# Kernel optimization log

Hardware: AMD Instinct MI355X
Metric: run time of the kernel (lower is better)

## Reference

```python
import jax, jax.numpy as jnp
import numpy as np

D = 512
H = 8
DH = D // H
HID = int(2 * D * 4.0 * (2.0 / 3.0))  # 2730, SwiGLU hidden


def _ln(x, g, b, eps=1e-5):
    m = jnp.mean(x, axis=-1, keepdims=True)
    v = jnp.mean(jnp.square(x - m), axis=-1, keepdims=True)
    return (x - m) * jax.lax.rsqrt(v + eps) * g + b


def _cross_attn(q_tok, kv_tok, ln_q_g, ln_q_b, ln_kv_g, ln_kv_b,
                Wqkv, bqkv, Wo, bo, Wp, bp):
    # q_tok: [B,Nq,D], kv_tok: [B,Nk,D]; Wqkv: [3D,D] fused in_proj (torch layout)
    B, Nq, _ = q_tok.shape
    Nk = kv_tok.shape[1]
    qn = _ln(q_tok, ln_q_g, ln_q_b)
    kvn = _ln(kv_tok, ln_kv_g, ln_kv_b)
    Wq, Wk, Wv = Wqkv[:D], Wqkv[D:2 * D], Wqkv[2 * D:]
    bq, bk, bv = bqkv[:D], bqkv[D:2 * D], bqkv[2 * D:]
    q = (qn @ Wq.T + bq).reshape(B, Nq, H, DH).transpose(0, 2, 1, 3)
    k = (kvn @ Wk.T + bk).reshape(B, Nk, H, DH).transpose(0, 2, 1, 3)
    v = (kvn @ Wv.T + bv).reshape(B, Nk, H, DH).transpose(0, 2, 1, 3)
    scores = jnp.einsum('bhqd,bhkd->bhqk', q, k) / jnp.sqrt(jnp.asarray(DH, q.dtype))
    attn = jax.nn.softmax(scores, axis=-1)
    ctx = jnp.einsum('bhqk,bhkd->bhqd', attn, v)
    ctx = ctx.transpose(0, 2, 1, 3).reshape(B, Nq, D)
    ctx = ctx @ Wo.T + bo          # MHA out_proj
    ctx = ctx @ Wp.T + bp          # CrossAttention extra out_proj
    return q_tok + ctx             # residual (dropout/droppath identity in eval)


def setup_inputs() -> dict:
    key = jax.random.key(0)
    ks = iter(jax.random.split(key, 32))
    s = 0.02
    inp = {
        'spatial_tokens': jax.random.normal(next(ks), (4, 4096, D), jnp.float32),
        'temporal_tokens': jax.random.normal(next(ks), (4, 512, D), jnp.float32),
    }
    for p in ('s', 't'):
        inp[f'{p}_ln_q_g'] = jnp.ones((D,), jnp.float32)
        inp[f'{p}_ln_q_b'] = jnp.zeros((D,), jnp.float32)
        inp[f'{p}_ln_kv_g'] = jnp.ones((D,), jnp.float32)
        inp[f'{p}_ln_kv_b'] = jnp.zeros((D,), jnp.float32)
        inp[f'{p}_Wqkv'] = jax.random.normal(next(ks), (3 * D, D), jnp.float32) * s
        inp[f'{p}_bqkv'] = jnp.zeros((3 * D,), jnp.float32)
        inp[f'{p}_Wo'] = jax.random.normal(next(ks), (D, D), jnp.float32) * s
        inp[f'{p}_bo'] = jnp.zeros((D,), jnp.float32)
        inp[f'{p}_Wp'] = jax.random.normal(next(ks), (D, D), jnp.float32) * s
        inp[f'{p}_bp'] = jnp.zeros((D,), jnp.float32)
    inp['mix_ln_g'] = jnp.ones((2 * D,), jnp.float32)
    inp['mix_ln_b'] = jnp.zeros((2 * D,), jnp.float32)
    inp['mix_Win'] = jax.random.normal(next(ks), (2 * HID, 2 * D), jnp.float32) * s
    inp['mix_bin'] = jnp.zeros((2 * HID,), jnp.float32)
    inp['mix_Wout'] = jax.random.normal(next(ks), (D, HID), jnp.float32) * s
    inp['mix_bout'] = jnp.zeros((D,), jnp.float32)
    return inp


def reference(spatial_tokens, temporal_tokens,
              s_ln_q_g, s_ln_q_b, s_ln_kv_g, s_ln_kv_b, s_Wqkv, s_bqkv, s_Wo, s_bo, s_Wp, s_bp,
              t_ln_q_g, t_ln_q_b, t_ln_kv_g, t_ln_kv_b, t_Wqkv, t_bqkv, t_Wo, t_bo, t_Wp, t_bp,
              mix_ln_g, mix_ln_b, mix_Win, mix_bin, mix_Wout, mix_bout):
    # 'st' (spatiotemporal) mode of CrossTransformer.forward
    s_ctx = _cross_attn(spatial_tokens, temporal_tokens,
                        s_ln_q_g, s_ln_q_b, s_ln_kv_g, s_ln_kv_b,
                        s_Wqkv, s_bqkv, s_Wo, s_bo, s_Wp, s_bp)
    t_ctx = _cross_attn(temporal_tokens, spatial_tokens,
                        t_ln_q_g, t_ln_q_b, t_ln_kv_g, t_ln_kv_b,
                        t_Wqkv, t_bqkv, t_Wo, t_bo, t_Wp, t_bp)
    t_mean = jnp.mean(t_ctx, axis=1, keepdims=True)  # [B,1,D]
    base = jnp.concatenate([s_ctx, jnp.broadcast_to(t_mean, s_ctx.shape)], axis=-1)  # [B,Ns,2D]
    h = _ln(base, mix_ln_g, mix_ln_b)
    uv = h @ mix_Win.T + mix_bin            # [B,Ns,2*HID]
    u, v = uv[..., :HID], uv[..., HID:]
    fused = (jax.nn.silu(u) * v) @ mix_Wout.T + mix_bout
    return s_ctx + fused
```

## Files before the change

kernel.cpp:

```cpp
#include <hip/hip_runtime.h>
#include <stdint.h>

typedef unsigned short u16;
typedef __bf16 bf16_t;
typedef bf16_t bf16x8 __attribute__((ext_vector_type(8)));
typedef float f32x4 __attribute__((ext_vector_type(4)));

__device__ __forceinline__ u16 f2b(float f) {
  union { float f; uint32_t u; } x; x.f = f;
  uint32_t r = x.u + 0x7fffu + ((x.u >> 16) & 1u);
  return (u16)(r >> 16);
}
__device__ __forceinline__ float b2f(u16 b) {
  union { uint32_t u; float f; } x; x.u = ((uint32_t)b) << 16;
  return x.f;
}

__device__ __forceinline__ void async16(const void* g, void* l) {
  auto gp = reinterpret_cast<__attribute__((address_space(1))) unsigned int*>(
      reinterpret_cast<uintptr_t>(g));
  auto lp = reinterpret_cast<__attribute__((address_space(3))) unsigned int*>(
      reinterpret_cast<uintptr_t>(l));
  __builtin_amdgcn_global_load_lds(gp, lp, 16, 0, 0);
}

__global__ __launch_bounds__(256) void pz_gemm_bt(
    const u16* __restrict__ A, const u16* __restrict__ B,
    const float* __restrict__ bias,
    const u16* __restrict__ residB, const float* __restrict__ residF,
    u16* __restrict__ Cb, float* __restrict__ Cf,
    int M, int N, int K, int ldA, int ldB, int ldC, int ldR,
    long aSH, long bSH, long cSH, long rSH, float alpha)
{
  __shared__ __align__(16) u16 sA[128 * 32];
  __shared__ __align__(16) u16 sB[128 * 32];

  const int tid = threadIdx.x;
  const int wave = tid >> 6, lane = tid & 63;
  const int lr = lane & 15, lg = lane >> 4;
  const int wm = wave >> 1, wn = wave & 1;
  const int z = blockIdx.z;

  const u16* Ab = A + (long)z * aSH;
  const u16* Bb = B + (long)z * bSH;
  const int m0 = blockIdx.y * 128;
  const int n0 = blockIdx.x * 128;

  const int srow = tid >> 2;
  const int sgk = (tid & 3) ^ ((tid >> 3) & 3);
  int ar0 = m0 + srow;      if (ar0 > M - 1) ar0 = M - 1;
  int ar1 = m0 + 64 + srow; if (ar1 > M - 1) ar1 = M - 1;
  int br0 = n0 + srow;      if (br0 > N - 1) br0 = N - 1;
  int br1 = n0 + 64 + srow; if (br1 > N - 1) br1 = N - 1;
  const u16* aP0 = Ab + (long)ar0 * ldA + sgk * 8;
  const u16* aP1 = Ab + (long)ar1 * ldA + sgk * 8;
  const u16* bP0 = Bb + (long)br0 * ldB + sgk * 8;
  const u16* bP1 = Bb + (long)br1 * ldB + sgk * 8;
  u16* sAw0 = sA + wave * 512;
  u16* sAw1 = sA + 2048 + wave * 512;
  u16* sBw0 = sB + wave * 512;
  u16* sBw1 = sB + 2048 + wave * 512;

  const int swz = (lr >> 1) & 3;
  int aoff[4], boff[4];
#pragma unroll
  for (int i = 0; i < 4; ++i) {
    aoff[i] = (wm * 64 + i * 16 + lr) * 32 + ((lg ^ swz) * 8);
    boff[i] = (wn * 64 + i * 16 + lr) * 32 + ((lg ^ swz) * 8);
  }

  f32x4 acc[4][4] = {};
  const int kiters = K >> 5;
  for (int kt = 0; kt < kiters; ++kt) {
    const int k0 = kt << 5;
    __syncthreads();
    async16(aP0 + k0, sAw0);
    async16(aP1 + k0, sAw1);
    async16(bP0 + k0, sBw0);
    async16(bP1 + k0, sBw1);
    __builtin_amdgcn_s_waitcnt(0x0f70);
    __syncthreads();

    bf16x8 af[4], bfr[4];
#pragma unroll
    for (int i = 0; i < 4; ++i) af[i] = *(const bf16x8*)(sA + aoff[i]);
#pragma unroll
    for (int i = 0; i < 4; ++i) bfr[i] = *(const bf16x8*)(sB + boff[i]);
#pragma unroll
    for (int i = 0; i < 4; ++i)
#pragma unroll
      for (int j = 0; j < 4; ++j)
        acc[i][j] = __builtin_amdgcn_mfma_f32_16x16x32_bf16(af[i], bfr[j], acc[i][j], 0, 0, 0);
  }

  const long coff = (long)z * cSH;
  const long roff = (long)z * rSH;
#pragma unroll
  for (int j = 0; j < 4; ++j) {
    const int n = n0 + wn * 64 + j * 16 + lr;
    if (n < N) {
      const float bv = bias ? bias[n] : 0.0f;
#pragma unroll
      for (int i = 0; i < 4; ++i) {
        const int mb = m0 + wm * 64 + i * 16 + lg * 4;
#pragma unroll
        for (int r = 0; r < 4; ++r) {
          const int m = mb + r;
          float v = alpha * acc[i][j][r] + bv;
          const long ri = roff + (long)m * ldR + n;
          if (residB) v += b2f(residB[ri]);
          if (residF) v += residF[ri];
          const long ci = coff + (long)m * ldC + n;
          if (Cb) Cb[ci] = f2b(v);
          if (Cf) Cf[ci] = v;
        }
      }
    }
  }
}

__global__ __launch_bounds__(256) void pz_sattn(
    const u16* __restrict__ Q, const u16* __restrict__ K,
    const u16* __restrict__ V, u16* __restrict__ O)
{
  __shared__ __align__(16) u16 sQ[32 * 64];
  __shared__ __align__(16) u16 sK[512 * 32];
  __shared__ float redm[32][4];
  __shared__ float reds[32][4];

  const int tid = threadIdx.x;
  const int wave = tid >> 6, lane = tid & 63;
  const int lr = lane & 15, lg = lane >> 4;
  const int z = blockIdx.z;
  const int b = z >> 3, h = z & 7;
  const int q0 = blockIdx.x * 32;

  const u16* Qb = Q + (long)b * 4096 * 512 + h * 64;
  const u16* Kb = K + (long)b * 512 * 1024 + h * 64;
  const u16* Vb = V + ((long)b * 8 + h) * (64L * 512);
  u16* Ob = O + (long)b * 4096 * 512 + h * 64;

  {
    const int qrow = wave * 8 + (lane >> 3);
    const int qcol = ((lane & 7) ^ (lane >> 3)) * 8;
    async16(Qb + (long)(q0 + qrow) * 512 + qcol, sQ + wave * 512);
  }
  const int krow = wave * 16 + (lane >> 2);
  const int kcol = ((lane & 3) ^ ((lane >> 3) & 3)) * 8;
  const u16* kP = Kb + (long)krow * 1024 + kcol;

  f32x4 acc[8][2] = {};
#pragma unroll
  for (int kk = 0; kk < 2; ++kk) {
    __syncthreads();
#pragma unroll
    for (int s = 0; s < 8; ++s)
      async16(kP + kk * 32 + (long)s * 64 * 1024, sK + s * 2048 + wave * 512);
    __builtin_amdgcn_s_waitcnt(0x0f70);
    __syncthreads();

    bf16x8 kf[8], qf[2];
#pragma unroll
    for (int kb = 0; kb < 8; ++kb) {
      const int n = wave * 128 + kb * 16 + lr;
      kf[kb] = *(const bf16x8*)(sK + n * 32 + ((lg ^ ((lr >> 1) & 3)) * 8));
    }
#pragma unroll
    for (int nq = 0; nq < 2; ++nq) {
      const int r = nq * 16 + lr;
      qf[nq] = *(const bf16x8*)(sQ + r * 64 + (((kk * 4 + lg) ^ (r & 7)) * 8));
    }
#pragma unroll
    for (int kb = 0; kb < 8; ++kb)
#pragma unroll
      for (int nq = 0; nq < 2; ++nq)
        acc[kb][nq] = __builtin_amdgcn_mfma_f32_16x16x32_bf16(kf[kb], qf[nq], acc[kb][nq], 0, 0, 0);
  }

  float mx0, mx1;
  {
    float m0 = acc[0][0][0], m1 = acc[0][1][0];
#pragma unroll
    for (int kb = 0; kb < 8; ++kb)
#pragma unroll
      for (int rg = 0; rg < 4; ++rg) {
        m0 = fmaxf(m0, acc[kb][0][rg]);
        m1 = fmaxf(m1, acc[kb][1][rg]);
      }
    m0 = fmaxf(m0, __shfl_xor(m0, 16, 64)); m0 = fmaxf(m0, __shfl_xor(m0, 32, 64));
    m1 = fmaxf(m1, __shfl_xor(m1, 16, 64)); m1 = fmaxf(m1, __shfl_xor(m1, 32, 64));
    mx0 = m0; mx1 = m1;
  }
  if (lane < 16) { redm[lr][wave] = mx0; redm[16 + lr][wave] = mx1; }
  __syncthreads();
  float inv[2];
#pragma unroll
  for (int nq = 0; nq < 2; ++nq) {
    const int q = nq * 16 + lr;
    const float m = fmaxf(fmaxf(redm[q][0], redm[q][1]), fmaxf(redm[q][2], redm[q][3]));
    float s = 0.0f;
#pragma unroll
    for (int kb = 0; kb < 8; ++kb)
#pragma unroll
      for (int rg = 0; rg < 4; ++rg) {
        const float e = __expf(0.125f * (acc[kb][nq][rg] - m));
        acc[kb][nq][rg] = e;
        s += e;
      }
    s += __shfl_xor(s, 16, 64);
    s += __shfl_xor(s, 32, 64);
    if (lane < 16) reds[q][wave] = s;
  }
  __syncthreads();
#pragma unroll
  for (int nq = 0; nq < 2; ++nq) {
    const int q = nq * 16 + lr;
    inv[nq] = 1.0f / (reds[q][0] + reds[q][1] + reds[q][2] + reds[q][3]);
  }

#pragma unroll
  for (int nq = 0; nq < 2; ++nq) {
    const int q = nq * 16 + lr;
#pragma unroll
    for (int kb = 0; kb < 8; ++kb) {
      ushort4 w;
      w.x = f2b(acc[kb][nq][0] * inv[nq]);
      w.y = f2b(acc[kb][nq][1] * inv[nq]);
      w.z = f2b(acc[kb][nq][2] * inv[nq]);
      w.w = f2b(acc[kb][nq][3] * inv[nq]);
      const int c16 = wave * 16 + kb * 2 + (lg >> 1);
      const int byteoff = q * 1024 + ((c16 ^ (q & 7)) * 16) + (lg & 1) * 8;
      *(ushort4*)((char*)sK + byteoff) = w;
    }
  }
  __syncthreads();

  const u16* vp = Vb + (long)(wave * 16 + lr) * 512;
  f32x4 opv[2] = {};
#pragma unroll
  for (int ks = 0; ks < 16; ++ks) {
    const bf16x8 bv = *(const bf16x8*)(vp + ks * 32 + lg * 8);
    bf16x8 pf[2];
#pragma unroll
    for (int mi = 0; mi < 2; ++mi) {
      const int r = mi * 16 + lr;
      pf[mi] = *(const bf16x8*)((char*)sK + r * 1024 + (((ks * 4 + lg) ^ (lr & 7)) * 16));
    }
#pragma unroll
    for (int mi = 0; mi < 2; ++mi)
      opv[mi] = __builtin_amdgcn_mfma_f32_16x16x32_bf16(pf[mi], bv, opv[mi], 0, 0, 0);
  }
#pragma unroll
  for (int mi = 0; mi < 2; ++mi)
#pragma unroll
    for (int rg = 0; rg < 4; ++rg) {
      const int q = q0 + mi * 16 + lg * 4 + rg;
      Ob[(long)q * 512 + wave * 16 + lr] = f2b(opv[mi][rg]);
    }
}

__global__ __launch_bounds__(256) void pz_tattn(
    const u16* __restrict__ Q,
    const u16* __restrict__ K,
    const u16* __restrict__ VT,
    u16* __restrict__ O)
{
  __shared__ __align__(16) u16 sQ[32 * 64];
  __shared__ __align__(16) u16 sK[512 * 32];
  __shared__ float redm[32][4];
  __shared__ float reds[32][4];
  __shared__ float m_run[32], l_run[32], alpha_sh[32];

  const int tid = threadIdx.x;
  const int wave = tid >> 6, lane = tid & 63;
  const int lr = lane & 15, lg = lane >> 4;
  const int z = blockIdx.z;
  const int b = z >> 3, h = z & 7;
  const int q0 = blockIdx.x * 32;

  const u16* Qb = Q + (long)b * 512 * 512 + h * 64;
  const u16* Kb = K + (long)b * 4096 * 1024 + h * 64;
  const u16* Vb = VT + (long)b * 512 * 4096 + (long)h * 64 * 4096;
  u16* Ob = O + (long)b * 512 * 512 + h * 64;

  if (tid < 32) { m_run[tid] = -3.0e38f; l_run[tid] = 0.0f; }

  {
    const int qrow = wave * 8 + (lane >> 3);
    const int qcol = ((lane & 7) ^ (lane >> 3)) * 8;
    async16(Qb + (long)(q0 + qrow) * 512 + qcol, sQ + wave * 512);
  }
  const int krow = wave * 16 + (lane >> 2);
  const int kcol = ((lane & 3) ^ ((lane >> 3) & 3)) * 8;

  f32x4 opv[2] = {};

  for (int kt = 0; kt < 8; ++kt) {
    const u16* kP = Kb + ((long)kt * 512 + krow) * 1024 + kcol;
    f32x4 acc[8][2] = {};
#pragma unroll
    for (int kk = 0; kk < 2; ++kk) {
      __syncthreads();
#pragma unroll
      for (int s = 0; s < 8; ++s)
        async16(kP + kk * 32 + (long)s * 64 * 1024, sK + s * 2048 + wave * 512);
      __builtin_amdgcn_s_waitcnt(0x0f70);
      __syncthreads();

      bf16x8 kf[8], qf[2];
#pragma unroll
      for (int kb = 0; kb < 8; ++kb) {
        const int n = wave * 128 + kb * 16 + lr;
        kf[kb] = *(const bf16x8*)(sK + n * 32 + ((lg ^ ((lr >> 1) & 3)) * 8));
      }
#pragma unroll
      for (int nq = 0; nq < 2; ++nq) {
        const int r = nq * 16 + lr;
        qf[nq] = *(const bf16x8*)(sQ + r * 64 + (((kk * 4 + lg) ^ (r & 7)) * 8));
      }
#pragma unroll
      for (int kb = 0; kb < 8; ++kb)
#pragma unroll
        for (int nq = 0; nq < 2; ++nq)
          acc[kb][nq] = __builtin_amdgcn_mfma_f32_16x16x32_bf16(kf[kb], qf[nq], acc[kb][nq], 0, 0, 0);
    }

#pragma unroll
    for (int nq = 0; nq < 2; ++nq) {
      float m = acc[0][nq][0];
#pragma unroll
      for (int kb = 0; kb < 8; ++kb)
#pragma unroll
        for (int rg = 0; rg < 4; ++rg) m = fmaxf(m, acc[kb][nq][rg]);
      m = fmaxf(m, __shfl_xor(m, 16, 64));
      m = fmaxf(m, __shfl_xor(m, 32, 64));
      if (lane < 16) redm[nq * 16 + lr][wave] = m;
    }
    __syncthreads();

#pragma unroll
    for (int nq = 0; nq < 2; ++nq) {
      const int q = nq * 16 + lr;
      const float mt = fmaxf(fmaxf(redm[q][0], redm[q][1]), fmaxf(redm[q][2], redm[q][3]));
      const float mn = fmaxf(m_run[q], mt);
      float s = 0.0f;
#pragma unroll
      for (int kb = 0; kb < 8; ++kb)
#pragma unroll
        for (int rg = 0; rg < 4; ++rg) {
          const float e = __expf(0.125f * (acc[kb][nq][rg] - mn));
          acc[kb][nq][rg] = e;
          s += e;
        }
      s += __shfl_xor(s, 16, 64);
      s += __shfl_xor(s, 32, 64);
      if (lane < 16) reds[q][wave] = s;
    }
    __syncthreads();

    if (tid < 32) {
      const int q = tid;
      const float mt = fmaxf(fmaxf(redm[q][0], redm[q][1]), fmaxf(redm[q][2], redm[q][3]));
      const float mo = m_run[q];
      const float mn = fmaxf(mo, mt);
      const float al = __expf(0.125f * (mo - mn));
      l_run[q] = l_run[q] * al + (reds[q][0] + reds[q][1] + reds[q][2] + reds[q][3]);
      m_run[q] = mn;
      alpha_sh[q] = al;
    }
#pragma unroll
    for (int nq = 0; nq < 2; ++nq) {
      const int q = nq * 16 + lr;
#pragma unroll
      for (int kb = 0; kb < 8; ++kb) {
        ushort4 w;
        w.x = f2b(acc[kb][nq][0]);
        w.y = f2b(acc[kb][nq][1]);
        w.z = f2b(acc[kb][nq][2]);
        w.w = f2b(acc[kb][nq][3]);
        const int c16 = wave * 16 + kb * 2 + (lg >> 1);
        const int byteoff = q * 1024 + ((c16 ^ (q & 7)) * 16) + (lg & 1) * 8;
        *(ushort4*)((char*)sK + byteoff) = w;
      }
    }
    __syncthreads();

#pragma unroll
    for (int mi = 0; mi < 2; ++mi)
#pragma unroll
      for (int rg = 0; rg < 4; ++rg)
        opv[mi][rg] *= alpha_sh[mi * 16 + lg * 4 + rg];

    const u16* vp = Vb + (long)(wave * 16 + lr) * 4096 + kt * 512;
#pragma unroll
    for (int ks = 0; ks < 16; ++ks) {
      const bf16x8 bv = *(const bf16x8*)(vp + ks * 32 + lg * 8);
      bf16x8 pf[2];
#pragma unroll
      for (int mi = 0; mi < 2; ++mi) {
        const int r = mi * 16 + lr;
        pf[mi] = *(const bf16x8*)((char*)sK + r * 1024 + (((ks * 4 + lg) ^ (lr & 7)) * 16));
      }
#pragma unroll
      for (int mi = 0; mi < 2; ++mi)
        opv[mi] = __builtin_amdgcn_mfma_f32_16x16x32_bf16(pf[mi], bv, opv[mi], 0, 0, 0);
    }
  }

#pragma unroll
  for (int mi = 0; mi < 2; ++mi)
#pragma unroll
    for (int rg = 0; rg < 4; ++rg) {
      const int qr = mi * 16 + lg * 4 + rg;
      Ob[(long)(q0 + qr) * 512 + wave * 16 + lr] = f2b(opv[mi][rg] * (1.0f / l_run[qr]));
    }
}

__global__ __launch_bounds__(256) void pz_gemm_uvgate(
    const u16* __restrict__ A, const u16* __restrict__ Bu, const u16* __restrict__ Bv,
    const float* __restrict__ biasU, const float* __restrict__ biasV,
    u16* __restrict__ G, int M, int N, int K, int ldA, int ldB, int ldG, int Npad)
{
  __shared__ __align__(16) u16 sA[2][128 * 32];
  __shared__ __align__(16) u16 sU[2][64 * 32];
  __shared__ __align__(16) u16 sV[2][64 * 32];

  const int tid = threadIdx.x;
  const int wave = tid >> 6, lane = tid & 63;
  const int lr = lane & 15, lg = lane >> 4;
  const int wm = wave >> 1, wn = wave & 1;
  const int m0 = blockIdx.y * 128;
  const int n0 = blockIdx.x * 64;

  const int srow = tid >> 2;
  const int sgk = (tid & 3) ^ ((tid >> 3) & 3);
  int ar0 = m0 + srow;      if (ar0 > M - 1) ar0 = M - 1;
  int ar1 = m0 + 64 + srow; if (ar1 > M - 1) ar1 = M - 1;
  int br  = n0 + srow;      if (br  > N - 1) br  = N - 1;
  const u16* aP0 = A + (long)ar0 * ldA + sgk * 8;
  const u16* aP1 = A + (long)ar1 * ldA + sgk * 8;
  const u16* uP  = Bu + (long)br * ldB + sgk * 8;
  const u16* vP  = Bv + (long)br * ldB + sgk * 8;

  auto stage = [&](int buf, int k0) {
    u16* a = sA[buf];
    u16* u = sU[buf];
    u16* v = sV[buf];
    async16(aP0 + k0, a + wave * 512);
    async16(aP1 + k0, a + 2048 + wave * 512);
    async16(uP + k0, u + wave * 512);
    async16(vP + k0, v + wave * 512);
  };

  const int swz = (lr >> 1) & 3;
  int aoff[4], boff[2];
#pragma unroll
  for (int i = 0; i < 4; ++i) aoff[i] = (wm * 64 + i * 16 + lr) * 32 + ((lg ^ swz) * 8);
#pragma unroll
  for (int j = 0; j < 2; ++j) boff[j] = (wn * 32 + j * 16 + lr) * 32 + ((lg ^ swz) * 8);

  f32x4 aU[4][2] = {}, aV[4][2] = {};
  const int kiters = K >> 5;

  stage(0, 0);
  __builtin_amdgcn_s_waitcnt(0x0f70);
  __syncthreads();

  int cur = 0;
  for (int kt = 0; kt < kiters; ++kt) {
    if (kt + 1 < kiters) stage(cur ^ 1, (kt + 1) << 5);

    const u16* sAc = sA[cur];
    const u16* sUc = sU[cur];
    const u16* sVc = sV[cur];
    bf16x8 af[4], uf[2], vf[2];
#pragma unroll
    for (int i = 0; i < 4; ++i) af[i] = *(const bf16x8*)(sAc + aoff[i]);
#pragma unroll
    for (int j = 0; j < 2; ++j) uf[j] = *(const bf16x8*)(sUc + boff[j]);
#pragma unroll
    for (int j = 0; j < 2; ++j) vf[j] = *(const bf16x8*)(sVc + boff[j]);
#pragma unroll
    for (int i = 0; i < 4; ++i)
#pragma unroll
      for (int j = 0; j < 2; ++j) {
        aU[i][j] = __builtin_amdgcn_mfma_f32_16x16x32_bf16(af[i], uf[j], aU[i][j], 0, 0, 0);
        aV[i][j] = __builtin_amdgcn_mfma_f32_16x16x32_bf16(af[i], vf[j], aV[i][j], 0, 0, 0);
      }

    __builtin_amdgcn_s_waitcnt(0x0f70);
    __syncthreads();
    cur ^= 1;
  }

#pragma unroll
  for (int j = 0; j < 2; ++j) {
    const int n = n0 + wn * 32 + j * 16 + lr;
    if (n < N) {
      const float bu = biasU[n], bv = biasV[n];
#pragma unroll
      for (int i = 0; i < 4; ++i) {
        const int mb = m0 + wm * 64 + i * 16 + lg * 4;
#pragma unroll
        for (int r = 0; r < 4; ++r) {
          const float u = aU[i][j][r] + bu;
          const float v = aV[i][j][r] + bv;
          G[(long)(mb + r) * ldG + n] = f2b((u / (1.0f + __expf(-u))) * v);
        }
      }
    } else if (n < Npad) {
#pragma unroll
      for (int i = 0; i < 4; ++i) {
        const int mb = m0 + wm * 64 + i * 16 + lg * 4;
#pragma unroll
        for (int r = 0; r < 4; ++r) G[(long)(mb + r) * ldG + n] = 0;
      }
    }
  }
}

__global__ __launch_bounds__(256) void pz_ln(const float* __restrict__ X, u16* __restrict__ O)
{
  __shared__ float sm[4], sq[4];
  const int tid = threadIdx.x;
  const long row = blockIdx.x;
  const float* x = X + row * 512;
  float a = x[tid], b = x[tid + 256];
  float s = a + b, q = a * a + b * b;
#pragma unroll
  for (int m = 32; m >= 1; m >>= 1) { s += __shfl_xor(s, m, 64); q += __shfl_xor(q, m, 64); }
  if ((tid & 63) == 0) { sm[tid >> 6] = s; sq[tid >> 6] = q; }
  __syncthreads();
  s = sm[0] + sm[1] + sm[2] + sm[3];
  q = sq[0] + sq[1] + sq[2] + sq[3];
  const float mean = s * (1.0f / 512.0f);
  const float rstd = rsqrtf(q * (1.0f / 512.0f) - mean * mean + 1e-5f);
  O[row * 512 + tid]       = f2b((a - mean) * rstd);
  O[row * 512 + tid + 256] = f2b((b - mean) * rstd);
}

__global__ __launch_bounds__(256) void pz_mix_ln(
    const u16* __restrict__ SC, const float* __restrict__ TM,
    const float* __restrict__ g, const float* __restrict__ b, u16* __restrict__ H)
{
  __shared__ float sm[4], sq[4];
  const int tid = threadIdx.x;
  const long row = blockIdx.x;
  const int bb = (int)(row >> 12);
  const u16* x0 = SC + row * 512;
  const float* x1 = TM + (long)bb * 512;
  float v0 = b2f(x0[tid]), v1 = b2f(x0[tid + 256]);
  float v2 = x1[tid], v3 = x1[tid + 256];
  float s = v0 + v1 + v2 + v3;
  float q = v0 * v0 + v1 * v1 + v2 * v2 + v3 * v3;
#pragma unroll
  for (int m = 32; m >= 1; m >>= 1) { s += __shfl_xor(s, m, 64); q += __shfl_xor(q, m, 64); }
  if ((tid & 63) == 0) { sm[tid >> 6] = s; sq[tid >> 6] = q; }
  __syncthreads();
  s = sm[0] + sm[1] + sm[2] + sm[3];
  q = sq[0] + sq[1] + sq[2] + sq[3];
  const float mean = s * (1.0f / 1024.0f);
  const float rstd = rsqrtf(q * (1.0f / 1024.0f) - mean * mean + 1e-5f);
  u16* hr = H + row * 1024;
  hr[tid]       = f2b((v0 - mean) * rstd * g[tid]       + b[tid]);
  hr[tid + 256] = f2b((v1 - mean) * rstd * g[tid + 256] + b[tid + 256]);
  hr[tid + 512] = f2b((v2 - mean) * rstd * g[tid + 512] + b[tid + 512]);
  hr[tid + 768] = f2b((v3 - mean) * rstd * g[tid + 768] + b[tid + 768]);
}

__global__ __launch_bounds__(256) void pz_transpose(
    const u16* __restrict__ S, u16* __restrict__ D, int Nk, int ldS, int colBase)
{
  __shared__ u16 t[64][65];
  const int z = blockIdx.z;
  const int nk0 = blockIdx.x * 64;
  const int tid = threadIdx.x;
  for (int i = tid; i < 4096; i += 256) {
    int r = i >> 6, d = i & 63;
    t[r][d] = S[(long)(nk0 + r) * ldS + colBase + z * 64 + d];
  }
  __syncthreads();
  for (int i = tid; i < 4096; i += 256) {
    int d = i >> 6, c = i & 63;
    D[((long)z * 64 + d) * Nk + nk0 + c] = t[c][d];
  }
}

__global__ __launch_bounds__(256) void pz_transpose_f2b(
    const float* __restrict__ S, u16* __restrict__ D, int Nk, int ldS)
{
  __shared__ u16 t[64][65];
  const int z = blockIdx.z;
  const int nk0 = blockIdx.x * 64;
  const int tid = threadIdx.x;
  for (int i = tid; i < 4096; i += 256) {
    int r = i >> 6, d = i & 63;
    t[r][d] = f2b(S[(long)(nk0 + r) * ldS + z * 64 + d]);
  }
  __syncthreads();
  for (int i = tid; i < 4096; i += 256) {
    int d = i >> 6, c = i & 63;
    D[((long)z * 64 + d) * Nk + nk0 + c] = t[c][d];
  }
}

__global__ __launch_bounds__(256) void pz_f2b(const float* __restrict__ s, u16* __restrict__ d, int n)
{
  int i = blockIdx.x * 256 + threadIdx.x;
  if (i < n) d[i] = f2b(s[i]);
}

__global__ __launch_bounds__(256) void pz_fold_qkv(
    const float* __restrict__ Ws, const float* __restrict__ Wt,
    const float* __restrict__ bs, const float* __restrict__ bt,
    const float* s_qg, const float* s_qb, const float* s_kg, const float* s_kb,
    const float* t_qg, const float* t_qb, const float* t_kg, const float* t_kb,
    u16* __restrict__ Wps, u16* __restrict__ Wpt, float* bps, float* bpt)
{
  __shared__ float sb[4];
  const int id = blockIdx.x;
  const int mat = (id >= 1536) ? 1 : 0;
  const int r = id - mat * 1536;
  const float* W = mat ? Wt : Ws;
  const float* bq = mat ? bt : bs;
  const float *g, *bl;
  if (!mat) { g = (r < 512) ? s_qg : s_kg; bl = (r < 512) ? s_qb : s_kb; }
  else      { g = (r < 512) ? t_qg : t_kg; bl = (r < 512) ? t_qb : t_kb; }
  u16* Wo_ = mat ? Wpt : Wps;
  float* bo_ = mat ? bpt : bps;
  float dot = 0.0f;
  for (int c = threadIdx.x; c < 512; c += 256) {
    float w = W[(long)r * 512 + c];
    Wo_[(long)r * 512 + c] = f2b(w * g[c]);
    dot += w * bl[c];
  }
#pragma unroll
  for (int m = 32; m >= 1; m >>= 1) dot += __shfl_xor(dot, m, 64);
  if ((threadIdx.x & 63) == 0) sb[threadIdx.x >> 6] = dot;
  __syncthreads();
  if (threadIdx.x == 0) bo_[r] = sb[0] + sb[1] + sb[2] + sb[3] + bq[r];
}

__global__ __launch_bounds__(256) void pz_fold_bc(
    const float* Wps_, const float* bos, const float* bps_,
    const float* Wpt_, const float* bot, const float* bpt_, float* bcs, float* bct)
{
  __shared__ float sb[4];
  const int id = blockIdx.x;
  const int mat = id >> 9, i = id & 511;
  const float* W = mat ? Wpt_ : Wps_;
  const float* bo = mat ? bot : bos;
  const float* bp = mat ? bpt_ : bps_;
  float* o = mat ? bct : bcs;
  float dot = 0.0f;
  for (int j = threadIdx.x; j < 512; j += 256) dot += W[(long)i * 512 + j] * bo[j];
#pragma unroll
  for (int m = 32; m >= 1; m >>= 1) dot += __shfl_xor(dot, m, 64);
  if ((threadIdx.x & 63) == 0) sb[threadIdx.x >> 6] = dot;
  __syncthreads();
  if (threadIdx.x == 0) o[i] = sb[0] + sb[1] + sb[2] + sb[3] + bp[i];
}

__global__ __launch_bounds__(256) void pz_pad_wout(const float* __restrict__ W, u16* __restrict__ D)
{
  const int idx = blockIdx.x * 256 + threadIdx.x;
  const int r = idx / 2816, c = idx - r * 2816;
  D[idx] = (c < 2730) ? f2b(W[(long)r * 2730 + c]) : (u16)0;
}

__global__ __launch_bounds__(256) void pz_tmean(const u16* __restrict__ T, float* __restrict__ O)
{
  const int b = blockIdx.y, tc = blockIdx.x, tid = threadIdx.x;
  const u16* base = T + (long)b * 512 * 512 + (long)tc * 32 * 512;
  float s0 = 0.0f, s1 = 0.0f;
#pragma unroll 4
  for (int t = 0; t < 32; ++t) { s0 += b2f(base[t * 512 + tid]); s1 += b2f(base[t * 512 + tid + 256]); }
  atomicAdd(&O[b * 512 + tid],       s0 * (1.0f / 512.0f));
  atomicAdd(&O[b * 512 + tid + 256], s1 * (1.0f / 512.0f));
}

__global__ void pz_diag(float* __restrict__ out, long n, float val)
{
  for (long i = (long)blockIdx.x * 256 + threadIdx.x; i < n; i += (long)gridDim.x * 256)
    out[i] = val;
}

extern "C" void kernel_launch(void* const* d_in, const int* in_sizes, int n_in,
                              void* d_out, int out_size, void* d_ws, size_t ws_size,
                              hipStream_t stream)
{
  (void)in_sizes; (void)n_in;
  const float* spat   = (const float*)d_in[0];
  const float* temp   = (const float*)d_in[1];
  const float* s_qg = (const float*)d_in[2],  * s_qb = (const float*)d_in[3];
  const float* s_kg = (const float*)d_in[4],  * s_kb = (const float*)d_in[5];
  const float* s_Wqkv = (const float*)d_in[6], * s_bqkv = (const float*)d_in[7];
  const float* s_Wo = (const float*)d_in[8],  * s_bo = (const float*)d_in[9];
  const float* s_Wp = (const float*)d_in[10], * s_bp = (const float*)d_in[11];
  const float* t_qg = (const float*)d_in[12], * t_qb = (const float*)d_in[13];
  const float* t_kg = (const float*)d_in[14], * t_kb = (const float*)d_in[15];
  const float* t_Wqkv = (const float*)d_in[16], * t_bqkv = (const float*)d_in[17];
  const float* t_Wo = (const float*)d_in[18], * t_bo = (const float*)d_in[19];
  const float* t_Wp = (const float*)d_in[20], * t_bp = (const float*)d_in[21];
  const float* mix_g = (const float*)d_in[22], * mix_b = (const float*)d_in[23];
  const float* mix_Win = (const float*)d_in[24], * mix_bin = (const float*)d_in[25];
  const float* mix_Wout = (const float*)d_in[26], * mix_bout = (const float*)d_in[27];
  float* out = (float*)d_out;

  char* ws = (char*)d_ws;
  size_t off = 0;
  auto take = [&](size_t n) { void* p = ws + off; off += (n + 255) & ~(size_t)255; return p; };

  u16* wq_s  = (u16*)take(1536L * 512 * 2);
  u16* wq_t  = (u16*)take(1536L * 512 * 2);
  u16* wc_s  = (u16*)take(512L * 512 * 2);
  u16* wc_t  = (u16*)take(512L * 512 * 2);
  u16* woutp = (u16*)take(512L * 2816 * 2);
  float* bqs = (float*)take(1536L * 4);
  float* bqt = (float*)take(1536L * 4);
  float* bcs = (float*)take(512L * 4);
  float* bct = (float*)take(512L * 4);
  u16* nhat_s = (u16*)take(16384L * 512 * 2);
  u16* nhat_t = (u16*)take(2048L * 512 * 2);
  u16* q_s  = (u16*)take(16384L * 512 * 2);
  u16* kv_s = (u16*)take(2048L * 1024 * 2);
  u16* q_t  = (u16*)take(2048L * 512 * 2);
  u16* kv_t = (u16*)take(16384L * 1024 * 2);
  char* Sreg = (char*)take(16777216 + 2097152 + 4194304);
  const size_t NEED = off;

  if (ws_size < NEED) {
    pz_diag<<<2048, 256, 0, stream>>>(out, (long)out_size, (float)(ws_size >> 20));
    return;
  }

  u16* Gbig = (u16*)(ws + off);
  const bool bigG = (ws_size >= off + 16384UL * 2816 * 2);

  u16* wtT  = (u16*)Sreg;
  u16* wpb  = (u16*)(Sreg + 524288);
  u16* vt_s = (u16*)Sreg;
  u16* vtc4 = (u16*)(Sreg + 2097152);
  u16* ctx_s = nhat_s;
  u16* ctx_t = nhat_t;
  u16* sctx  = q_s;
  u16* tctx  = kv_s;
  float* tmean = (float*)q_t;
  u16* hbuf  = kv_t;
  u16* gchunk = (u16*)Sreg;
  u16* winb   = (u16*)nhat_s;

  auto gemm = [&](const u16* A, const u16* B, const float* bias,
                  const u16* residB, const float* residF, u16* Cb, float* Cf,
                  int M, int N, int K, int ldA, int ldB, int ldC, int ldR,
                  long aSH, long bSH, long cSH, long rSH, int Z, float alpha) {
    dim3 g((N + 127) / 128, M / 128, Z);
    pz_gemm_bt<<<g, dim3(256), 0, stream>>>(A, B, bias, residB, residF, Cb, Cf,
        M, N, K, ldA, ldB, ldC, ldR, aSH, bSH, cSH, rSH, alpha);
  };

  pz_fold_qkv<<<3072, 256, 0, stream>>>(s_Wqkv, t_Wqkv, s_bqkv, t_bqkv,
      s_qg, s_qb, s_kg, s_kb, t_qg, t_qb, t_kg, t_kb, wq_s, wq_t, bqs, bqt);
  pz_transpose_f2b<<<dim3(8, 1, 8), 256, 0, stream>>>(s_Wo, wtT, 512, 512);
  pz_f2b<<<1024, 256, 0, stream>>>(s_Wp, wpb, 512 * 512);
  gemm(wpb, wtT, nullptr, nullptr, nullptr, wc_s, nullptr,
       512, 512, 512, 512, 512, 512, 0, 0, 0, 0, 0, 1, 1.0f);
  pz_transpose_f2b<<<dim3(8, 1, 8), 256, 0, stream>>>(t_Wo, wtT, 512, 512);
  pz_f2b<<<1024, 256, 0, stream>>>(t_Wp, wpb, 512 * 512);
  gemm(wpb, wtT, nullptr, nullptr, nullptr, wc_t, nullptr,
       512, 512, 512, 512, 512, 512, 0, 0, 0, 0, 0, 1, 1.0f);
  pz_fold_bc<<<1024, 256, 0, stream>>>(s_Wp, s_bo, s_bp, t_Wp, t_bo, t_bp, bcs, bct);
  pz_pad_wout<<<5632, 256, 0, stream>>>(mix_Wout, woutp);

  pz_ln<<<16384, 256, 0, stream>>>(spat, nhat_s);
  pz_ln<<<2048, 256, 0, stream>>>(temp, nhat_t);

  gemm(nhat_s, wq_s,           bqs,       nullptr, nullptr, q_s,  nullptr,
       16384, 512,  512, 512, 512, 512,  0, 0,0,0,0, 1, 1.0f);
  gemm(nhat_t, wq_s + 512*512, bqs + 512, nullptr, nullptr, kv_s, nullptr,
       2048,  1024, 512, 512, 512, 1024, 0, 0,0,0,0, 1, 1.0f);
  gemm(nhat_t, wq_t,           bqt,       nullptr, nullptr, q_t,  nullptr,
       2048,  512,  512, 512, 512, 512,  0, 0,0,0,0, 1, 1.0f);
  gemm(nhat_s, wq_t + 512*512, bqt + 512, nullptr, nullptr, kv_t, nullptr,
       16384, 1024, 512, 512, 512, 1024, 0, 0,0,0,0, 1, 1.0f);

  for (int b = 0; b < 4; ++b)
    pz_transpose<<<dim3(8, 1, 8), 256, 0, stream>>>(kv_s + (long)b * 512 * 1024,
        vt_s + (long)b * 8 * 64 * 512, 512, 1024, 512);
  for (int b = 0; b < 4; ++b)
    pz_transpose<<<dim3(64, 1, 8), 256, 0, stream>>>(kv_t + (long)b * 4096 * 1024,
        vtc4 + (long)b * 512 * 4096, 4096, 1024, 512);

  pz_sattn<<<dim3(128, 1, 32), 256, 0, stream>>>(q_s, kv_s, vt_s, ctx_s);
  pz_tattn<<<dim3(16, 1, 32), 256, 0, stream>>>(q_t, kv_t, vtc4, ctx_t);

  gemm(ctx_s, wc_s, bcs, nullptr, spat, sctx, nullptr,
       16384, 512, 512, 512, 512, 512, 512, 0,0,0,0, 1, 1.0f);
  gemm(ctx_t, wc_t, bct, nullptr, temp, tctx, nullptr,
       2048,  512, 512, 512, 512, 512, 512, 0,0,0,0, 1, 1.0f);

  (void)hipMemsetAsync(tmean, 0, 4L * 512 * sizeof(float), stream);
  pz_tmean<<<dim3(16, 4), 256, 0, stream>>>(tctx, tmean);
  pz_mix_ln<<<16384, 256, 0, stream>>>(sctx, tmean, mix_g, mix_b, hbuf);

  pz_f2b<<<21840, 256, 0, stream>>>(mix_Win, winb, 5460 * 1024);

  if (bigG) {
    pz_gemm_uvgate<<<dim3(44, 128), 256, 0, stream>>>(hbuf, winb, winb + 2730L * 1024,
        mix_bin, mix_bin + 2730, Gbig, 16384, 2730, 1024, 1024, 1024, 2816, 2816);
    gemm(Gbig, woutp, mix_bout, sctx, nullptr, nullptr, out,
         16384, 512, 2816, 2816, 2816, 512, 512, 0,0,0,0, 1, 1.0f);
  } else {
    for (int c = 0; c < 4; ++c) {
      const u16* Ah = hbuf + (long)c * 4096 * 1024;
      pz_gemm_uvgate<<<dim3(44, 32), 256, 0, stream>>>(Ah, winb, winb + 2730L * 1024,
          mix_bin, mix_bin + 2730, gchunk, 4096, 2730, 1024, 1024, 1024, 2816, 2816);
      gemm(gchunk, woutp, mix_bout, sctx + (long)c * 4096 * 512, nullptr, nullptr,
           out + (long)c * 4096 * 512,
           4096, 512, 2816, 2816, 2816, 512, 512, 0,0,0,0, 1, 1.0f);
    }
  }
}
```

Baseline: 917.9 us.

## Double-buffer generic GEMM and triple-buffer SwiGLU gate GEMM with vmcnt waits

The generic bt GEMM moves from single-buffered LDS staging to a double-buffered pipeline that prefetches the next K tile while the current tile runs its MFMAs. The SwiGLU up/gate GEMM goes from two to three LDS buffers in one flat array, keeping two tiles in flight and waiting with partial vmcnt counts instead of draining all loads each iteration. This aims to hide global-load latency behind compute. In exchange it uses more LDS per block, which may reduce occupancy, and the hand-written waitcnt and barrier ordering is fragile.

```diff
diff --git a/kernel.cpp b/kernel.cpp
--- a/kernel.cpp
+++ b/kernel.cpp
@@ -32,8 +32,8 @@
     int M, int N, int K, int ldA, int ldB, int ldC, int ldR,
     long aSH, long bSH, long cSH, long rSH, float alpha)
 {
-  __shared__ __align__(16) u16 sA[128 * 32];
-  __shared__ __align__(16) u16 sB[128 * 32];
+  __shared__ __align__(16) u16 sA[2][128 * 32];
+  __shared__ __align__(16) u16 sB[2][128 * 32];
 
   const int tid = threadIdx.x;
   const int wave = tid >> 6, lane = tid & 63;
@@ -56,10 +56,13 @@
   const u16* aP1 = Ab + (long)ar1 * ldA + sgk * 8;
   const u16* bP0 = Bb + (long)br0 * ldB + sgk * 8;
   const u16* bP1 = Bb + (long)br1 * ldB + sgk * 8;
-  u16* sAw0 = sA + wave * 512;
-  u16* sAw1 = sA + 2048 + wave * 512;
-  u16* sBw0 = sB + wave * 512;
-  u16* sBw1 = sB + 2048 + wave * 512;
+
+  auto stage = [&](int buf, int k0) {
+    async16(aP0 + k0, sA[buf] + wave * 512);
+    async16(aP1 + k0, sA[buf] + 2048 + wave * 512);
+    async16(bP0 + k0, sB[buf] + wave * 512);
+    async16(bP1 + k0, sB[buf] + 2048 + wave * 512);
+  };
 
   const int swz = (lr >> 1) & 3;
   int aoff[4], boff[4];
@@ -71,26 +74,31 @@
 
   f32x4 acc[4][4] = {};
   const int kiters = K >> 5;
+
+  stage(0, 0);
+  __builtin_amdgcn_s_waitcnt(0x0f70);
+  __syncthreads();
+
+  int cur = 0;
   for (int kt = 0; kt < kiters; ++kt) {
-    const int k0 = kt << 5;
-    __syncthreads();
-    async16(aP0 + k0, sAw0);
-    async16(aP1 + k0, sAw1);
-    async16(bP0 + k0, sBw0);
-    async16(bP1 + k0, sBw1);
+    if (kt + 1 < kiters) stage(cur ^ 1, (kt + 1) << 5);
+
+    const u16* sAc = sA[cur];
+    const u16* sBc = sB[cur];
+    bf16x8 af[4], bfr[4];
+#pragma unroll
+    for (int i = 0; i < 4; ++i) af[i] = *(const bf16x8*)(sAc + aoff[i]);
+#pragma unroll
+    for (int i = 0; i < 4; ++i) bfr[i] = *(const bf16x8*)(sBc + boff[i]);
+#pragma unroll
+    for (int i = 0; i < 4; ++i)
+#pragma unroll
+      for (int j = 0; j < 4; ++j)
+        acc[i][j] = __builtin_amdgcn_mfma_f32_16x16x32_bf16(af[i], bfr[j], acc[i][j], 0, 0, 0);
+
     __builtin_amdgcn_s_waitcnt(0x0f70);
     __syncthreads();
-
-    bf16x8 af[4], bfr[4];
-#pragma unroll
-    for (int i = 0; i < 4; ++i) af[i] = *(const bf16x8*)(sA + aoff[i]);
-#pragma unroll
-    for (int i = 0; i < 4; ++i) bfr[i] = *(const bf16x8*)(sB + boff[i]);
-#pragma unroll
-    for (int i = 0; i < 4; ++i)
-#pragma unroll
-      for (int j = 0; j < 4; ++j)
-        acc[i][j] = __builtin_amdgcn_mfma_f32_16x16x32_bf16(af[i], bfr[j], acc[i][j], 0, 0, 0);
+    cur ^= 1;
   }
 
   const long coff = (long)z * cSH;
@@ -421,9 +429,7 @@
     const float* __restrict__ biasU, const float* __restrict__ biasV,
     u16* __restrict__ G, int M, int N, int K, int ldA, int ldB, int ldG, int Npad)
 {
-  __shared__ __align__(16) u16 sA[2][128 * 32];
-  __shared__ __align__(16) u16 sU[2][64 * 32];
-  __shared__ __align__(16) u16 sV[2][64 * 32];
+  __shared__ __align__(16) u16 sAll[3 * 8192];
 
   const int tid = threadIdx.x;
   const int wave = tid >> 6, lane = tid & 63;
@@ -443,13 +449,11 @@
   const u16* vP  = Bv + (long)br * ldB + sgk * 8;
 
   auto stage = [&](int buf, int k0) {
-    u16* a = sA[buf];
-    u16* u = sU[buf];
-    u16* v = sV[buf];
-    async16(aP0 + k0, a + wave * 512);
-    async16(aP1 + k0, a + 2048 + wave * 512);
-    async16(uP + k0, u + wave * 512);
-    async16(vP + k0, v + wave * 512);
+    u16* b = sAll + buf * 8192;
+    async16(aP0 + k0, b + wave * 512);
+    async16(aP1 + k0, b + 2048 + wave * 512);
+    async16(uP + k0, b + 4096 + wave * 512);
+    async16(vP + k0, b + 6144 + wave * 512);
   };
 
   const int swz = (lr >> 1) & 3;
@@ -463,23 +467,28 @@
   const int kiters = K >> 5;
 
   stage(0, 0);
-  __builtin_amdgcn_s_waitcnt(0x0f70);
-  __syncthreads();
+  if (kiters > 1) stage(1, 32);
 
   int cur = 0;
   for (int kt = 0; kt < kiters; ++kt) {
-    if (kt + 1 < kiters) stage(cur ^ 1, (kt + 1) << 5);
-
-    const u16* sAc = sA[cur];
-    const u16* sUc = sU[cur];
-    const u16* sVc = sV[cur];
+    if (kt + 2 < kiters) {
+      const int nx = (cur + 2 >= 3) ? cur - 1 : cur + 2;
+      stage(nx, (kt + 2) << 5);
+    }
+    if (kt + 2 < kiters)      asm volatile("s_waitcnt vmcnt(8)" ::: "memory");
+    else if (kt + 1 < kiters) asm volatile("s_waitcnt vmcnt(4)" ::: "memory");
+    else                      asm volatile("s_waitcnt vmcnt(0)" ::: "memory");
+    __builtin_amdgcn_s_barrier();
+    asm volatile("" ::: "memory");
+
+    const u16* base = sAll + cur * 8192;
     bf16x8 af[4], uf[2], vf[2];
 #pragma unroll
-    for (int i = 0; i < 4; ++i) af[i] = *(const bf16x8*)(sAc + aoff[i]);
-#pragma unroll
-    for (int j = 0; j < 2; ++j) uf[j] = *(const bf16x8*)(sUc + boff[j]);
-#pragma unroll
-    for (int j = 0; j < 2; ++j) vf[j] = *(const bf16x8*)(sVc + boff[j]);
+    for (int i = 0; i < 4; ++i) af[i] = *(const bf16x8*)(base + aoff[i]);
+#pragma unroll
+    for (int j = 0; j < 2; ++j) uf[j] = *(const bf16x8*)(base + 4096 + boff[j]);
+#pragma unroll
+    for (int j = 0; j < 2; ++j) vf[j] = *(const bf16x8*)(base + 6144 + boff[j]);
 #pragma unroll
     for (int i = 0; i < 4; ++i)
 #pragma unroll
@@ -488,9 +497,9 @@
         aV[i][j] = __builtin_amdgcn_mfma_f32_16x16x32_bf16(af[i], vf[j], aV[i][j], 0, 0, 0);
       }
 
-    __builtin_amdgcn_s_waitcnt(0x0f70);
-    __syncthreads();
-    cur ^= 1;
+    asm volatile("" ::: "memory");
+    __builtin_amdgcn_s_barrier();
+    cur = (cur + 1 == 3) ? 0 : cur + 1;
   }
 
 #pragma unroll
```

Result: faster. 871.0 us (-5.1%).
